# Kernel optimization log

Measured on AMD Instinct MI355X. Metric: run time of the kernel, lower is better.

Reference implementation:

```python
import jax, jax.numpy as jnp
import numpy as np
from jax.ops import segment_sum

GRID = 32        # cells per axis; offset grid is (GRID+1)^3
T = 48           # number of accepted MC topologies
N_PTS = 131072

# 12 cube edges: base (lower) corner offset and axis the edge runs along.
# e0..3: x/y edges of z=0 face, e4..7: same at z=1, e8..11: vertical z edges.
EDGE_BASE = np.array([[0,0,0],[1,0,0],[0,1,0],[0,0,0],
                      [0,0,1],[1,0,1],[0,1,1],[0,0,1],
                      [0,0,0],[1,0,0],[1,1,0],[0,1,0]], dtype=np.int32)
EDGE_AXIS = np.array([0,1,0,1, 0,1,0,1, 2,2,2,2], dtype=np.int32)
EDGE_DIR  = np.eye(3, dtype=np.float32)[EDGE_AXIS]          # [12,3] unit dirs


def _dot(u, v):
    return jnp.sum(u * v, axis=-1)


def _safe_div(n, d, eps=1e-12):
    return n / jnp.where(jnp.abs(d) > eps, d, eps)


def _point_tri_dist_sq(p, a, b, c):
    """Squared distance from p to triangle (a,b,c); Ericson closest-point
    algorithm with full vertex/edge/interior region clamping, vectorized.
    p broadcasts against a/b/c over leading dims; last dim is xyz."""
    ab = b - a; ac = c - a; ap = p - a
    d1 = _dot(ab, ap); d2 = _dot(ac, ap)
    bp = p - b; d3 = _dot(ab, bp); d4 = _dot(ac, bp)
    cp = p - c; d5 = _dot(ab, cp); d6 = _dot(ac, cp)
    vc = d1 * d4 - d3 * d2
    vb = d5 * d2 - d1 * d6
    va = d3 * d6 - d5 * d4
    v_ab = _safe_div(d1, d1 - d3)
    w_ac = _safe_div(d2, d2 - d6)
    w_bc = _safe_div(d4 - d3, (d4 - d3) + (d5 - d6))
    inv = _safe_div(jnp.ones_like(va), va + vb + vc)
    v_in = vb * inv; w_in = vc * inv
    q = a + ab * v_in[..., None] + ac * w_in[..., None]                      # interior
    q = jnp.where(((va <= 0) & ((d4 - d3) >= 0) & ((d5 - d6) >= 0))[..., None],
                  b + (c - b) * w_bc[..., None], q)                          # edge BC
    q = jnp.where(((vb <= 0) & (d2 >= 0) & (d6 <= 0))[..., None],
                  a + ac * w_ac[..., None], q)                               # edge AC
    q = jnp.where(((d6 >= 0) & (d5 <= d6))[..., None], c, q)                 # vertex C
    q = jnp.where(((vc <= 0) & (d1 >= 0) & (d3 <= 0))[..., None],
                  a + ab * v_ab[..., None], q)                               # edge AB
    q = jnp.where(((d3 >= 0) & (d4 <= d3))[..., None], b, q)                 # vertex B
    q = jnp.where(((d1 <= 0) & (d2 <= 0))[..., None], a, q)                  # vertex A
    diff = p - q
    return _dot(diff, diff)


def setup_inputs() -> dict:
    key = jax.random.key(0)
    k1, k2, k3 = jax.random.split(key, 3)
    offset = jax.random.uniform(k1, (3, GRID + 1, GRID + 1, GRID + 1), dtype=jnp.float32)
    points = jax.random.uniform(k2, (N_PTS, 3), dtype=jnp.float32) * GRID
    tri_table = jax.random.randint(k3, (T, 3, 3), 0, 12, dtype=jnp.int32)
    return {"offset": offset, "points": points, "tri_table": tri_table}


def reference(offset, points, tri_table):
    edge_base_i = jnp.asarray(EDGE_BASE)                 # [12,3] int
    edge_base_f = jnp.asarray(EDGE_BASE, dtype=offset.dtype)
    edge_dir = jnp.asarray(EDGE_DIR, dtype=offset.dtype)
    edge_axis = jnp.asarray(EDGE_AXIS)

    cell = jnp.clip(jnp.floor(points).astype(jnp.int32), 0, GRID - 1)   # [N,3]
    local = points - cell.astype(points.dtype)                          # [N,3] in [0,1)^3

    # grid index of each edge's base corner -> edge offset parameter t in [0,1]
    gidx = cell[:, None, :] + edge_base_i[None, :, :]                   # [N,12,3]
    t = offset[edge_axis[None, :], gidx[..., 0], gidx[..., 1], gidx[..., 2]]  # [N,12]
    verts = edge_base_f[None] + edge_dir[None] * t[..., None]           # [N,12,3] local coords

    tri = verts[:, tri_table]                                           # [N,T,3tri,3vert,3]
    a = tri[:, :, :, 0, :]; b = tri[:, :, :, 1, :]; c = tri[:, :, :, 2, :]
    p = local[:, None, None, :]                                         # [N,1,1,3]
    d2 = _point_tri_dist_sq(p, a, b, c)                                 # [N,T,3]
    d_min = jnp.min(d2, axis=-1)                                        # [N,T]

    cell_id = (cell[:, 0] * GRID + cell[:, 1]) * GRID + cell[:, 2]      # [N]
    distances_full = segment_sum(d_min, cell_id, num_segments=GRID ** 3)  # [GRID^3, T]
    return distances_full
```

## Files before the change

### kernel.cpp

```cpp
#include <hip/hip_runtime.h>

#define GRID 32
#define NT 48
#define BLK 256
#define SPLIT 16
#define PPB (BLK / SPLIT)
#define NCELLS (GRID * GRID * GRID)
#define CAP 32
#define CAP2 16

#define EDGE_PACK ( (0ULL<<0) | (9ULL<<5) | (2ULL<<10) | (8ULL<<15) | \
                    (4ULL<<20) | (13ULL<<25) | (6ULL<<30) | (12ULL<<35) | \
                    (16ULL<<40) | (17ULL<<45) | (19ULL<<50) | (18ULL<<55) )

__device__ __forceinline__ float tri_dist_gram(float AA, float AB, float AC,
                                               float BB, float BC, float CC) {
    float d1 = AA - AB, d2 = AA - AC;
    float d3 = AB - BB, d4 = AB - BC;
    float d5 = AC - BC, d6 = AC - CC;
    float d43 = BB - BC;
    float d56 = CC - BC;
    float vc = d1 * d4 - d3 * d2;
    float vb = d5 * d2 - d1 * d6;
    float va = d3 * d6 - d5 * d4;

    bool cbc = (va <= 0.f) & (d43 >= 0.f) & (d56 >= 0.f);
    bool cac = (vb <= 0.f) & (d2 >= 0.f) & (d6 <= 0.f);
    bool ccc = (d6 >= 0.f) & (d5 <= d6);
    bool cab = (vc <= 0.f) & (d1 >= 0.f) & (d3 <= 0.f);
    bool cbb = (d3 >= 0.f) & (d4 <= d3);
    bool caa = (d1 <= 0.f) & (d2 <= 0.f);

    float nv = vb, nw = vc, den = va + vb + vc;
    nw = cbc ? d43 : nw;  den = cbc ? d43 + d56 : den;
    nv = cac ? 0.f : nv;  nw = cac ? d2  : nw;  den = cac ? d2 - d6 : den;
    nv = cab ? d1  : nv;  nw = cab ? 0.f : nw;  den = cab ? d1 - d3 : den;
    bool mode = cbc & !cac & !cab;

    float dd  = (fabsf(den) > 1e-12f) ? den : 1e-12f;
    float inv = __builtin_amdgcn_rcpf(dd);
    float vp = nv * inv;
    float wp = nw * inv;
    float u = mode ? 0.f : 1.f - vp - wp;
    float v = mode ? 1.f - wp : vp;
    float e1 = fmaf(AC, wp, fmaf(AB, v, AA * u));
    float e2 = fmaf(BC, wp, fmaf(BB, v, AB * u));
    float e3 = fmaf(CC, wp, fmaf(BC, v, AC * u));
    float r  = fmaf(wp, e3, fmaf(v, e2, u * e1));
    r = (ccc & !cab) ? CC : r;
    r = cbb ? BB : r;
    r = caa ? AA : r;
    return r;
}

template<bool SLOT>
__global__ __launch_bounds__(BLK) void eval_kernel(
    const float* __restrict__ offset,
    const float* __restrict__ points,
    const int*   __restrict__ tri_table,
    int*         __restrict__ cnt,
    int*         __restrict__ wlist,
    int*         __restrict__ ovf_cnt,
    int*         __restrict__ ovf,
    float*       __restrict__ dmin,
    float*       __restrict__ dmin_ovf,
    int n)
{
    __shared__ float4 v_s[PPB * 13];
    __shared__ float  gram[PPB * 144];
    __shared__ int2   goff[NT * 3];
    __shared__ int    pos_s[PPB];

    const int tid = threadIdx.x;
    const int g   = blockIdx.x * BLK + tid;
    const int pt  = g >> 4;
    const int grp = tid & 15;
    const int pl  = tid >> 4;
    const bool active = (pt < n);

    if (tid < NT * 3) {
        int i = tri_table[tid * 3 + 0];
        int j = tri_table[tid * 3 + 1];
        int k = tri_table[tid * 3 + 2];
        int o0 = (i * 13) | ((i * 12 + j) << 8) | ((i * 12 + k) << 16);
        int o1 = (j * 13) | ((j * 12 + k) << 8) | ((k * 13) << 16);
        goff[tid] = make_int2(o0, o1);
    }

    float4 vi = make_float4(0.f, 0.f, 0.f, 0.f);
    if (active) {
        float px = points[pt * 3 + 0];
        float py = points[pt * 3 + 1];
        float pz = points[pt * 3 + 2];
        int cx = min(max((int)floorf(px), 0), GRID - 1);
        int cy = min(max((int)floorf(py), 0), GRID - 1);
        int cz = min(max((int)floorf(pz), 0), GRID - 1);
        if (grp == 0) {
            int cellid = ((cx * GRID) + cy) * GRID + cz;
            int pos = atomicAdd(&cnt[cellid], 1);
            if (SLOT) {
                int base;
                if (pos < CAP2) base = cellid * CAP2 + pos;
                else { int e = atomicAdd(ovf_cnt, 1); ovf[e] = cellid;
                       base = 0x40000000 | e; }
                pos_s[pl] = base;
            } else {
                if (pos < CAP) wlist[cellid * CAP + pos] = pt;
                else { int e = atomicAdd(ovf_cnt, 1); ovf[e] = (cellid << 17) | pt; }
            }
        }
        if (grp < 12) {
            float lx = px - (float)cx;
            float ly = py - (float)cy;
            float lz = pz - (float)cz;
            unsigned nib = (unsigned)(EDGE_PACK >> (5 * grp)) & 31u;
            int gx = cx + (int)(nib & 1u);
            int gy = cy + (int)((nib >> 1) & 1u);
            int gz = cz + (int)((nib >> 2) & 1u);
            int ax = (int)(nib >> 3);
            float t = offset[((ax * 33 + gx) * 33 + gy) * 33 + gz];
            float vx = (ax == 0) ? t : (float)(nib & 1u);
            float vy = (ax == 1) ? t : (float)((nib >> 1) & 1u);
            float vz = (ax == 2) ? t : (float)((nib >> 2) & 1u);
            vi = make_float4(lx - vx, ly - vy, lz - vz, 0.0f);
            v_s[pl * 13 + grp] = vi;
        }
    }
    __syncthreads();
    if (active && grp < 12) {
        float* gp = &gram[pl * 144];
        int j = grp;
#pragma unroll
        for (int d = 0; d < 7; d++) {
            float4 vj = v_s[pl * 13 + j];
            float dv = fmaf(vi.z, vj.z, fmaf(vi.y, vj.y, vi.x * vj.x));
            gp[grp * 12 + j] = dv;
            gp[j * 12 + grp] = dv;
            j = (j == 11) ? 0 : j + 1;
        }
    }
    __syncthreads();
    if (!active) return;

    const float* gp = &gram[pl * 144];
    const int2* gofft = &goff[grp * 9];
    float dm[3];
#pragma unroll
    for (int r = 0; r < 3; r++) {
        float dmn;
#pragma unroll
        for (int k = 0; k < 3; k++) {
            int2 o = gofft[r * 3 + k];
            float AA = gp[o.x & 255];
            float AB = gp[(o.x >> 8) & 255];
            float AC = gp[(unsigned)o.x >> 16];
            float BB = gp[o.y & 255];
            float BC = gp[(o.y >> 8) & 255];
            float CC = gp[(unsigned)o.y >> 16];
            float d = tri_dist_gram(AA, AB, AC, BB, BC, CC);
            dmn = (k == 0) ? d : fminf(dmn, d);
        }
        dm[r] = dmn;
    }
    float* dp;
    if (SLOT) {
        int base = pos_s[pl];
        dp = (base & 0x40000000)
               ? &dmin_ovf[(size_t)(base & 0x3FFFFFFF) * NT + grp * 3]
               : &dmin[(size_t)base * NT + grp * 3];
    } else {
        dp = &dmin[(size_t)pt * NT + grp * 3];
    }
    dp[0] = dm[0]; dp[1] = dm[1]; dp[2] = dm[2];
}

__global__ __launch_bounds__(BLK) void reduce_slot_kernel(
    const int*   __restrict__ cnt,
    const int*   __restrict__ ovf_cnt,
    const int*   __restrict__ ovf,
    const float* __restrict__ dmin,
    const float* __restrict__ dmin_ovf,
    float*       __restrict__ out)
{
    const int tid  = threadIdx.x;
    const int grp  = tid & 15;
    const int pl   = tid >> 4;
    const int cell = blockIdx.x * PPB + pl;

    const int c = min(cnt[cell], CAP2);
    const float* bp = &dmin[(size_t)cell * CAP2 * NT + grp * 3];
    float s0 = 0.f, s1 = 0.f, s2 = 0.f;
    for (int i = 0; i < c; i++) {
        s0 += bp[0]; s1 += bp[1]; s2 += bp[2];
        bp += NT;
    }
    const int movf = *ovf_cnt;
    for (int e = 0; e < movf; e++) {
        if (ovf[e] == cell) {
            const float* dp = &dmin_ovf[(size_t)e * NT + grp * 3];
            s0 += dp[0]; s1 += dp[1]; s2 += dp[2];
        }
    }
    float* op = &out[cell * NT + grp * 3];
    op[0] = s0; op[1] = s1; op[2] = s2;
}

__global__ __launch_bounds__(BLK) void reduce_kernel(
    const int*   __restrict__ cnt,
    const int*   __restrict__ wlist,
    const int*   __restrict__ ovf_cnt,
    const int*   __restrict__ ovf,
    const float* __restrict__ dmin,
    float*       __restrict__ out)
{
    const int tid  = threadIdx.x;
    const int grp  = tid & 15;
    const int pl   = tid >> 4;
    const int cell = blockIdx.x * PPB + pl;

    const int c = min(cnt[cell], CAP);
    const int* wl = &wlist[cell * CAP];
    float s0 = 0.f, s1 = 0.f, s2 = 0.f;
    for (int i = 0; i < c; i++) {
        int pt = wl[i];
        const float* dp = &dmin[(size_t)pt * NT + grp * 3];
        s0 += dp[0]; s1 += dp[1]; s2 += dp[2];
    }
    const int movf = *ovf_cnt;
    for (int e = 0; e < movf; e++) {
        int v = ovf[e];
        if ((v >> 17) == cell) {
            int pt = v & 0x1FFFF;
            const float* dp = &dmin[(size_t)pt * NT + grp * 3];
            s0 += dp[0]; s1 += dp[1]; s2 += dp[2];
        }
    }
    float* op = &out[cell * NT + grp * 3];
    op[0] = s0; op[1] = s1; op[2] = s2;
}

__global__ __launch_bounds__(BLK) void ptd_kernel(
    const float* __restrict__ offset,
    const float* __restrict__ points,
    const int*   __restrict__ tri_table,
    float*       __restrict__ out,
    int n)
{
    __shared__ float4 v_s[PPB * 13];
    __shared__ float  gram[PPB * 144];
    __shared__ int2   goff[NT * 3];

    const int tid = threadIdx.x;
    const int g   = blockIdx.x * BLK + tid;
    const int pt  = g >> 4;
    const int grp = tid & 15;
    const int pl  = tid >> 4;
    const bool active = (pt < n);

    if (tid < NT * 3) {
        int i = tri_table[tid * 3 + 0];
        int j = tri_table[tid * 3 + 1];
        int k = tri_table[tid * 3 + 2];
        int o0 = (i * 13) | ((i * 12 + j) << 8) | ((i * 12 + k) << 16);
        int o1 = (j * 13) | ((j * 12 + k) << 8) | ((k * 13) << 16);
        goff[tid] = make_int2(o0, o1);
    }

    float4 vi = make_float4(0.f, 0.f, 0.f, 0.f);
    int cx = 0, cy = 0, cz = 0;
    if (active) {
        float px = points[pt * 3 + 0];
        float py = points[pt * 3 + 1];
        float pz = points[pt * 3 + 2];
        cx = min(max((int)floorf(px), 0), GRID - 1);
        cy = min(max((int)floorf(py), 0), GRID - 1);
        cz = min(max((int)floorf(pz), 0), GRID - 1);
        if (grp < 12) {
            float lx = px - (float)cx;
            float ly = py - (float)cy;
            float lz = pz - (float)cz;
            unsigned nib = (unsigned)(EDGE_PACK >> (5 * grp)) & 31u;
            int gx = cx + (int)(nib & 1u);
            int gy = cy + (int)((nib >> 1) & 1u);
            int gz = cz + (int)((nib >> 2) & 1u);
            int ax = (int)(nib >> 3);
            float t = offset[((ax * 33 + gx) * 33 + gy) * 33 + gz];
            float vx = (ax == 0) ? t : (float)(nib & 1u);
            float vy = (ax == 1) ? t : (float)((nib >> 1) & 1u);
            float vz = (ax == 2) ? t : (float)((nib >> 2) & 1u);
            vi = make_float4(lx - vx, ly - vy, lz - vz, 0.0f);
            v_s[pl * 13 + grp] = vi;
        }
    }
    __syncthreads();
    if (active && grp < 12) {
        float* gp = &gram[pl * 144];
        int j = grp;
#pragma unroll
        for (int d = 0; d < 7; d++) {
            float4 vj = v_s[pl * 13 + j];
            float dv = fmaf(vi.z, vj.z, fmaf(vi.y, vj.y, vi.x * vj.x));
            gp[grp * 12 + j] = dv;
            gp[j * 12 + grp] = dv;
            j = (j == 11) ? 0 : j + 1;
        }
    }
    __syncthreads();
    if (!active) return;

    const float* gp = &gram[pl * 144];
    float* outp = out + ((((cx * GRID) + cy) * GRID + cz) * NT);
    const int2* gofft = &goff[grp * 9];
#pragma unroll
    for (int r = 0; r < 3; r++) {
        float dmn;
#pragma unroll
        for (int k = 0; k < 3; k++) {
            int2 o = gofft[r * 3 + k];
            float AA = gp[o.x & 255];
            float AB = gp[(o.x >> 8) & 255];
            float AC = gp[(unsigned)o.x >> 16];
            float BB = gp[o.y & 255];
            float BC = gp[(o.y >> 8) & 255];
            float CC = gp[(unsigned)o.y >> 16];
            float d = tri_dist_gram(AA, AB, AC, BB, BC, CC);
            dmn = (k == 0) ? d : fminf(dmn, d);
        }
        atomicAdd(&outp[grp * 3 + r], dmn);
    }
}

extern "C" void kernel_launch(void* const* d_in, const int* in_sizes, int n_in,
                              void* d_out, int out_size, void* d_ws, size_t ws_size,
                              hipStream_t stream) {
    const float* offset    = (const float*)d_in[0];
    const float* points    = (const float*)d_in[1];
    const int*   tri_table = (const int*)d_in[2];
    float* out = (float*)d_out;
    int n = in_sizes[1] / 3;

    const size_t CNT_BYTES = (size_t)NCELLS * 4;
    const size_t OVFC_OFF  = CNT_BYTES;
    const size_t OVF_OFF   = CNT_BYTES + 128;
    const size_t TAIL_OFF  = (OVF_OFF + (size_t)n * 4 + 255) & ~(size_t)255;

    const size_t DMIN2_BYTES = (size_t)NCELLS * CAP2 * NT * 4;
    const size_t DOVF_OFF    = TAIL_OFF + DMIN2_BYTES;
    const size_t WS_SLOT     = DOVF_OFF + (size_t)n * NT * 4;

    const size_t WL_BYTES = (size_t)NCELLS * CAP * 4;
    const size_t DMIN_OFF = TAIL_OFF + WL_BYTES;
    const size_t WS_FB    = DMIN_OFF + (size_t)n * NT * 4;

    char* ws = (char*)d_ws;
    int* cnt     = (int*)(ws);
    int* ovf_cnt = (int*)(ws + OVFC_OFF);
    int* ovf     = (int*)(ws + OVF_OFF);

    long total = (long)n * SPLIT;
    int blocks = (int)((total + BLK - 1) / BLK);

    if (ws_size >= WS_SLOT) {
        float* dmin2    = (float*)(ws + TAIL_OFF);
        float* dmin_ovf = (float*)(ws + DOVF_OFF);
        hipMemsetAsync(ws, 0, OVF_OFF, stream);
        eval_kernel<true><<<blocks, BLK, 0, stream>>>(
            offset, points, tri_table, cnt, nullptr, ovf_cnt, ovf,
            dmin2, dmin_ovf, n);
        reduce_slot_kernel<<<NCELLS / PPB, BLK, 0, stream>>>(
            cnt, ovf_cnt, ovf, dmin2, dmin_ovf, out);
    } else if (ws_size >= WS_FB) {
        int*   wlist = (int*)(ws + TAIL_OFF);
        float* dmin  = (float*)(ws + DMIN_OFF);
        hipMemsetAsync(ws, 0, OVF_OFF, stream);
        eval_kernel<false><<<blocks, BLK, 0, stream>>>(
            offset, points, tri_table, cnt, wlist, ovf_cnt, ovf,
            dmin, nullptr, n);
        reduce_kernel<<<NCELLS / PPB, BLK, 0, stream>>>(
            cnt, wlist, ovf_cnt, ovf, dmin, out);
    } else {
        hipMemsetAsync(d_out, 0, (size_t)out_size * sizeof(float), stream);
        ptd_kernel<<<blocks, BLK, 0, stream>>>(offset, points, tri_table, out, n);
    }
}
```

Baseline: 112.5 us.

## Replace block barriers with per-wave goff tables in eval kernel

Each wavefront now builds its own copy of the triangle offset table in shared memory. The two __syncthreads barriers in eval_kernel are removed on the assumption that a point's 16 threads and its gram data sit inside one wave. It also adds a minimum-blocks hint of 8 to launch_bounds. This saves block-wide synchronisation but leaves no explicit intra-wave LDS fence, so correctness depends on wave execution semantics; it also raises shared memory use and may limit registers.

```diff
diff --git a/kernel.cpp b/kernel.cpp
--- a/kernel.cpp
+++ b/kernel.cpp
@@ -5,9 +5,11 @@
 #define BLK 256
 #define SPLIT 16
 #define PPB (BLK / SPLIT)
+#define NWAVE (BLK / 64)
 #define NCELLS (GRID * GRID * GRID)
 #define CAP 32
 #define CAP2 16
+#define GSTRIDE 144
 
 #define EDGE_PACK ( (0ULL<<0) | (9ULL<<5) | (2ULL<<10) | (8ULL<<15) | \
                     (4ULL<<20) | (13ULL<<25) | (6ULL<<30) | (12ULL<<35) | \
@@ -54,7 +56,7 @@
 }
 
 template<bool SLOT>
-__global__ __launch_bounds__(BLK) void eval_kernel(
+__global__ __launch_bounds__(BLK, 8) void eval_kernel(
     const float* __restrict__ offset,
     const float* __restrict__ points,
     const int*   __restrict__ tri_table,
@@ -67,24 +69,31 @@
     int n)
 {
     __shared__ float4 v_s[PPB * 13];
-    __shared__ float  gram[PPB * 144];
-    __shared__ int2   goff[NT * 3];
+    __shared__ float  gram[PPB * GSTRIDE];
+    __shared__ int2   goff[NWAVE * NT * 3];
     __shared__ int    pos_s[PPB];
 
-    const int tid = threadIdx.x;
-    const int g   = blockIdx.x * BLK + tid;
-    const int pt  = g >> 4;
-    const int grp = tid & 15;
-    const int pl  = tid >> 4;
+    const int tid  = threadIdx.x;
+    const int g    = blockIdx.x * BLK + tid;
+    const int pt   = g >> 4;
+    const int grp  = tid & 15;
+    const int pl   = tid >> 4;
+    const int wid  = tid >> 6;
+    const int lane = tid & 63;
     const bool active = (pt < n);
 
-    if (tid < NT * 3) {
-        int i = tri_table[tid * 3 + 0];
-        int j = tri_table[tid * 3 + 1];
-        int k = tri_table[tid * 3 + 2];
-        int o0 = (i * 13) | ((i * 12 + j) << 8) | ((i * 12 + k) << 16);
-        int o1 = (j * 13) | ((j * 12 + k) << 8) | ((k * 13) << 16);
-        goff[tid] = make_int2(o0, o1);
+    if (lane < NT) {
+        int2* gw = &goff[wid * (NT * 3)];
+        const int t = lane;
+#pragma unroll
+        for (int k = 0; k < 3; k++) {
+            int e  = t * 3 + k;
+            int i  = tri_table[e * 3 + 0];
+            int j  = tri_table[e * 3 + 1];
+            int kk = tri_table[e * 3 + 2];
+            gw[e] = make_int2((i * 13) | ((i * 12 + j) << 8) | ((i * 12 + kk) << 16),
+                              (j * 13) | ((j * 12 + kk) << 8) | ((kk * 13) << 16));
+        }
     }
 
     float4 vi = make_float4(0.f, 0.f, 0.f, 0.f);
@@ -126,9 +135,8 @@
             v_s[pl * 13 + grp] = vi;
         }
     }
-    __syncthreads();
     if (active && grp < 12) {
-        float* gp = &gram[pl * 144];
+        float* gp = &gram[pl * GSTRIDE];
         int j = grp;
 #pragma unroll
         for (int d = 0; d < 7; d++) {
@@ -139,11 +147,10 @@
             j = (j == 11) ? 0 : j + 1;
         }
     }
-    __syncthreads();
     if (!active) return;
 
-    const float* gp = &gram[pl * 144];
-    const int2* gofft = &goff[grp * 9];
+    const float* gp = &gram[pl * GSTRIDE];
+    const int2* gofft = &goff[wid * (NT * 3) + grp * 9];
     float dm[3];
 #pragma unroll
     for (int r = 0; r < 3; r++) {
@@ -247,7 +254,7 @@
     int n)
 {
     __shared__ float4 v_s[PPB * 13];
-    __shared__ float  gram[PPB * 144];
+    __shared__ float  gram[PPB * GSTRIDE];
     __shared__ int2   goff[NT * 3];
 
     const int tid = threadIdx.x;
@@ -261,9 +268,8 @@
         int i = tri_table[tid * 3 + 0];
         int j = tri_table[tid * 3 + 1];
         int k = tri_table[tid * 3 + 2];
-        int o0 = (i * 13) | ((i * 12 + j) << 8) | ((i * 12 + k) << 16);
-        int o1 = (j * 13) | ((j * 12 + k) << 8) | ((k * 13) << 16);
-        goff[tid] = make_int2(o0, o1);
+        goff[tid] = make_int2((i * 13) | ((i * 12 + j) << 8) | ((i * 12 + k) << 16),
+                              (j * 13) | ((j * 12 + k) << 8) | ((k * 13) << 16));
     }
 
     float4 vi = make_float4(0.f, 0.f, 0.f, 0.f);
@@ -294,7 +300,7 @@
     }
     __syncthreads();
     if (active && grp < 12) {
-        float* gp = &gram[pl * 144];
+        float* gp = &gram[pl * GSTRIDE];
         int j = grp;
 #pragma unroll
         for (int d = 0; d < 7; d++) {
@@ -308,7 +314,7 @@
     __syncthreads();
     if (!active) return;
 
-    const float* gp = &gram[pl * 144];
+    const float* gp = &gram[pl * GSTRIDE];
     float* outp = out + ((((cx * GRID) + cy) * GRID + cz) * NT);
     const int2* gofft = &goff[grp * 9];
 #pragma unroll
```

Result: no change. 112.5 us (+0.0%).
